# Optimization experiments

Measured on AMD Instinct MI355X. Metric: run time of the kernel, lower is better.

## Reference

```python
import jax, jax.numpy as jnp
import numpy as np

EPS = 1e-6

def setup_inputs() -> dict:
    key = jax.random.key(0)
    k1, k2, k3 = jax.random.split(key, 3)
    B, D, V = 8, 4096, 32000
    hidden_states = jax.random.normal(k1, (B, D), dtype=jnp.float32)
    norm_weight = jax.random.normal(k2, (D,), dtype=jnp.float32)
    lm_head_weight = jax.random.normal(k3, (V, D), dtype=jnp.float32) * (D ** -0.5)
    return {"hidden_states": hidden_states, "norm_weight": norm_weight,
            "lm_head_weight": lm_head_weight}

def reference(hidden_states, norm_weight, lm_head_weight):
    # RMSNorm: x * rsqrt(mean(x^2) + eps) * gamma
    var = jnp.mean(jnp.square(hidden_states), axis=-1, keepdims=True)
    h = hidden_states * jax.lax.rsqrt(var + EPS) * norm_weight  # [B, D]
    # vocab projection (GEMV per row): logits [B, V]
    logits = jnp.einsum('bd,vd->bv', h, lm_head_weight)
    # top-1 token, matching torch.topk(logits.float(), 1) -> indices [B, 1]
    token = jnp.argmax(logits.astype(jnp.float32), axis=-1, keepdims=True)
    return token
```

## Files before the change

kernel.cpp:

```cpp
#include <hip/hip_runtime.h>
#include <stdint.h>


#define D 4096
#define BATCH 8
#define VOCAB 32000
#define VT 4
#define NGROUPS (VOCAB / VT)
#define NBLK 2000
#define EPS 1e-6f

typedef unsigned long long u64;
typedef float f32x4 __attribute__((ext_vector_type(4)));

__global__ __launch_bounds__(256) void rmsnorm_k(const float* __restrict__ x,
                                                 const float* __restrict__ g,
                                                 float* __restrict__ h) {
    const int b = blockIdx.x;
    const int t = threadIdx.x;
    const int wave = t >> 6, lane = t & 63;
    const float* xr = x + b * D;

    f32x4 xv[4];
    float s = 0.f;
#pragma unroll
    for (int i = 0; i < 4; ++i) {
        xv[i] = *(const f32x4*)(xr + i * 1024 + t * 4);
        s += xv[i].x * xv[i].x + xv[i].y * xv[i].y + xv[i].z * xv[i].z + xv[i].w * xv[i].w;
    }
#pragma unroll
    for (int m = 1; m < 64; m <<= 1) s += __shfl_xor(s, m, 64);

    __shared__ float wsum[4];
    if (lane == 0) wsum[wave] = s;
    __syncthreads();
    const float tot = wsum[0] + wsum[1] + wsum[2] + wsum[3];
    const float rs = rsqrtf(tot * (1.f / (float)D) + EPS);

#pragma unroll
    for (int i = 0; i < 4; ++i) {
        const int d = i * 1024 + t * 4;
        const f32x4 gv = *(const f32x4*)(g + d);
        f32x4 o;
        o.x = xv[i].x * rs * gv.x;
        o.y = xv[i].y * rs * gv.y;
        o.z = xv[i].z * rs * gv.z;
        o.w = xv[i].w * rs * gv.w;
        *(f32x4*)(h + b * D + d) = o;
    }
}

__global__ __launch_bounds__(256) void gemv_argmax_k(const float* __restrict__ W,
                                                     const float* __restrict__ h,
                                                     u64* __restrict__ partial) {
    const int lane = threadIdx.x & 63;
    const int wave = threadIdx.x >> 6;
    const int grp = blockIdx.x * 4 + wave;
    const int v0 = grp * VT;
    const float* Wb = W + (size_t)v0 * D;

    float acc[32];
#pragma unroll
    for (int i = 0; i < 32; ++i) acc[i] = 0.f;

    f32x4 bufA[VT], bufB[VT];
    const int dl = lane * 4;

#define LOADW(BUF, c)                                                           \
    {                                                                           \
        const int _d = (c) * 256 + dl;                                          \
        _Pragma("unroll")                                                       \
        for (int vi = 0; vi < VT; ++vi)                                         \
            BUF[vi] = __builtin_nontemporal_load((const f32x4*)(Wb + vi * D + _d)); \
    }

#define COMPUTE(BUF, c)                                                         \
    {                                                                           \
        const int _d = (c) * 256 + dl;                                          \
        _Pragma("unroll")                                                       \
        for (int b = 0; b < 8; ++b) {                                           \
            const f32x4 hv = *(const f32x4*)(h + b * D + _d);                   \
            _Pragma("unroll")                                                   \
            for (int vi = 0; vi < VT; ++vi)                                     \
                acc[b * VT + vi] += BUF[vi].x * hv.x + BUF[vi].y * hv.y +       \
                                    BUF[vi].z * hv.z + BUF[vi].w * hv.w;        \
        }                                                                       \
    }

    LOADW(bufA, 0)
#pragma unroll 1
    for (int c = 0; c < 16; c += 2) {
        LOADW(bufB, c + 1)
        COMPUTE(bufA, c)
        LOADW(bufA, (c + 2 < 16 ? c + 2 : 15))
        COMPUTE(bufB, c + 1)
    }
#undef LOADW
#undef COMPUTE

#pragma unroll
    for (int s = 0; s < 5; ++s) {
        const int m = 1 << s;
        const bool bit = (lane & m) != 0;
#pragma unroll
        for (int u = 0; u < (32 >> (s + 1)); ++u) {
            const float a = acc[2 * u];
            const float c2 = acc[2 * u + 1];
            const float keep = bit ? c2 : a;
            const float send = bit ? a : c2;
            acc[u] = keep + __shfl_xor(send, m, 64);
        }
    }
    float logit = acc[0] + __shfl_xor(acc[0], 32, 64);

    const int vidx = v0 + (lane & 3);
    const uint32_t fb = __float_as_uint(logit);
    const uint32_t key = (fb & 0x80000000u) ? ~fb : (fb | 0x80000000u);
    u64 best = ((u64)key << 32) | (uint32_t)(~(uint32_t)vidx);

#pragma unroll
    for (int m = 1; m <= 2; m <<= 1) {
        const u64 o = __shfl_xor(best, m, 64);
        if (o > best) best = o;
    }
    {
        const u64 o = __shfl_xor(best, 32, 64);
        if (o > best) best = o;
    }

    __shared__ u64 lb[4][8];
    if (lane < 32 && (lane & 3) == 0) lb[wave][lane >> 2] = best;
    __syncthreads();
    if (threadIdx.x < 8) {
        const u64 m0 = lb[0][threadIdx.x], m1 = lb[1][threadIdx.x];
        const u64 m2 = lb[2][threadIdx.x], m3 = lb[3][threadIdx.x];
        const u64 a = m0 > m1 ? m0 : m1;
        const u64 b2 = m2 > m3 ? m2 : m3;
        partial[(size_t)blockIdx.x * 8 + threadIdx.x] = a > b2 ? a : b2;
    }
}

__global__ __launch_bounds__(512) void finalize_k(const u64* __restrict__ partial,
                                                  int* __restrict__ out, int nblk) {
    const int b = threadIdx.x >> 6;
    const int lane = threadIdx.x & 63;
    u64 best = 0ull;
    for (int p = lane; p < nblk; p += 64) {
        const u64 x = partial[(size_t)p * 8 + b];
        if (x > best) best = x;
    }
#pragma unroll
    for (int m = 1; m < 64; m <<= 1) {
        const u64 o = __shfl_xor(best, m, 64);
        if (o > best) best = o;
    }
    if (lane == 0) out[b] = (int)(~(uint32_t)best);
}

extern "C" void kernel_launch(void* const* d_in, const int* in_sizes, int n_in,
                              void* d_out, int out_size, void* d_ws, size_t ws_size,
                              hipStream_t stream) {
    const float* x = (const float*)d_in[0];
    const float* g = (const float*)d_in[1];
    const float* W = (const float*)d_in[2];
    int* out = (int*)d_out;

    float* h = (float*)d_ws;
    u64* partial = (u64*)((char*)d_ws + BATCH * D * sizeof(float));

    rmsnorm_k<<<BATCH, 256, 0, stream>>>(x, g, h);
    gemv_argmax_k<<<NBLK, 256, 0, stream>>>(W, h, partial);
    finalize_k<<<1, 512, 0, stream>>>(partial, out, NBLK);
}
```

Baseline: 135.8 us.

## Make GEMV-argmax persistent with 1024-thread blocks and hidden states staged in LDS

Replaces the 2000-block, one-group-per-wave launch with 256 persistent blocks of 16 waves. Each wave loops over vocab groups in a grid-stride pattern and keeps a running best (logit, index). Each block first copies all 8×4096 normalized hidden states (128 KB) into shared memory so the inner product reads h from LDS instead of global/L2. The cost is a large per-block LDS copy and only one block per CU. The __launch_bounds__(1024, 4) hint asks for far more resident waves than the LDS allows, which may squeeze the register budget and cause spills.

```diff
diff --git a/kernel.cpp b/kernel.cpp
--- a/kernel.cpp
+++ b/kernel.cpp
@@ -7,7 +7,9 @@
 #define VOCAB 32000
 #define VT 4
 #define NGROUPS (VOCAB / VT)
-#define NBLK 2000
+#define NBLK 256
+#define WPB 16
+#define NWAVES (NBLK * WPB)
 #define EPS 1e-6f
 
 typedef unsigned long long u64;
@@ -50,73 +52,93 @@
     }
 }
 
-__global__ __launch_bounds__(256) void gemv_argmax_k(const float* __restrict__ W,
-                                                     const float* __restrict__ h,
-                                                     u64* __restrict__ partial) {
-    const int lane = threadIdx.x & 63;
-    const int wave = threadIdx.x >> 6;
-    const int grp = blockIdx.x * 4 + wave;
-    const int v0 = grp * VT;
-    const float* Wb = W + (size_t)v0 * D;
+__global__ __launch_bounds__(1024, 4) void gemv_argmax_k(const float* __restrict__ W,
+                                                         const float* __restrict__ h,
+                                                         u64* __restrict__ partial) {
+    extern __shared__ float hs[];
+    const int t = threadIdx.x;
 
-    float acc[32];
+    {
+        const f32x4* src = (const f32x4*)h;
+        f32x4* dst = (f32x4*)hs;
 #pragma unroll
-    for (int i = 0; i < 32; ++i) acc[i] = 0.f;
+        for (int i = 0; i < 8; ++i) dst[i * 1024 + t] = src[i * 1024 + t];
+    }
+    __syncthreads();
+
+    const int lane = t & 63;
+    const int wave = t >> 6;
+    const int wid = blockIdx.x * WPB + wave;
+    const int dl = lane * 4;
+
+    u64 best = 0ull;
 
     f32x4 bufA[VT], bufB[VT];
-    const int dl = lane * 4;
 
-#define LOADW(BUF, c)                                                           \
-    {                                                                           \
-        const int _d = (c) * 256 + dl;                                          \
-        _Pragma("unroll")                                                       \
-        for (int vi = 0; vi < VT; ++vi)                                         \
-            BUF[vi] = __builtin_nontemporal_load((const f32x4*)(Wb + vi * D + _d)); \
+#define LOADW(BUF, WB, c)                                                          \
+    {                                                                              \
+        const int _d = (c) * 256 + dl;                                             \
+        _Pragma("unroll")                                                          \
+        for (int vi = 0; vi < VT; ++vi)                                            \
+            BUF[vi] = __builtin_nontemporal_load((const f32x4*)((WB) + vi * D + _d)); \
     }
 
-#define COMPUTE(BUF, c)                                                         \
-    {                                                                           \
-        const int _d = (c) * 256 + dl;                                          \
-        _Pragma("unroll")                                                       \
-        for (int b = 0; b < 8; ++b) {                                           \
-            const f32x4 hv = *(const f32x4*)(h + b * D + _d);                   \
-            _Pragma("unroll")                                                   \
-            for (int vi = 0; vi < VT; ++vi)                                     \
-                acc[b * VT + vi] += BUF[vi].x * hv.x + BUF[vi].y * hv.y +       \
-                                    BUF[vi].z * hv.z + BUF[vi].w * hv.w;        \
-        }                                                                       \
+#define COMPUTE(BUF, c)                                                            \
+    {                                                                              \
+        const int _d = (c) * 256 + dl;                                             \
+        _Pragma("unroll")                                                          \
+        for (int b = 0; b < 8; ++b) {                                              \
+            const f32x4 hv = *(const f32x4*)(hs + b * D + _d);                     \
+            _Pragma("unroll")                                                      \
+            for (int vi = 0; vi < VT; ++vi)                                        \
+                acc[b * VT + vi] += BUF[vi].x * hv.x + BUF[vi].y * hv.y +          \
+                                    BUF[vi].z * hv.z + BUF[vi].w * hv.w;           \
+        }                                                                          \
     }
 
-    LOADW(bufA, 0)
 #pragma unroll 1
-    for (int c = 0; c < 16; c += 2) {
-        LOADW(bufB, c + 1)
-        COMPUTE(bufA, c)
-        LOADW(bufA, (c + 2 < 16 ? c + 2 : 15))
-        COMPUTE(bufB, c + 1)
+    for (int grp = wid; grp < NGROUPS; grp += NWAVES) {
+        const float* Wb = W + (size_t)grp * (VT * D);
+
+        float acc[32];
+#pragma unroll
+        for (int i = 0; i < 32; ++i) acc[i] = 0.f;
+
+        LOADW(bufA, Wb, 0)
+#pragma unroll 1
+        for (int c = 0; c <= 12; c += 2) {
+            LOADW(bufB, Wb, c + 1)
+            COMPUTE(bufA, c)
+            LOADW(bufA, Wb, c + 2)
+            COMPUTE(bufB, c + 1)
+        }
+        LOADW(bufB, Wb, 15)
+        COMPUTE(bufA, 14)
+        COMPUTE(bufB, 15)
+
+#pragma unroll
+        for (int s = 0; s < 5; ++s) {
+            const int m = 1 << s;
+            const bool bit = (lane & m) != 0;
+#pragma unroll
+            for (int u = 0; u < (32 >> (s + 1)); ++u) {
+                const float a = acc[2 * u];
+                const float c2 = acc[2 * u + 1];
+                const float keep = bit ? c2 : a;
+                const float send = bit ? a : c2;
+                acc[u] = keep + __shfl_xor(send, m, 64);
+            }
+        }
+        const float logit = acc[0] + __shfl_xor(acc[0], 32, 64);
+
+        const int vidx = grp * VT + (lane & 3);
+        const uint32_t fb = __float_as_uint(logit);
+        const uint32_t key = (fb & 0x80000000u) ? ~fb : (fb | 0x80000000u);
+        const u64 pk = ((u64)key << 32) | (uint32_t)(~(uint32_t)vidx);
+        if (pk > best) best = pk;
     }
 #undef LOADW
 #undef COMPUTE
-
-#pragma unroll
-    for (int s = 0; s < 5; ++s) {
-        const int m = 1 << s;
-        const bool bit = (lane & m) != 0;
-#pragma unroll
-        for (int u = 0; u < (32 >> (s + 1)); ++u) {
-            const float a = acc[2 * u];
-            const float c2 = acc[2 * u + 1];
-            const float keep = bit ? c2 : a;
-            const float send = bit ? a : c2;
-            acc[u] = keep + __shfl_xor(send, m, 64);
-        }
-    }
-    float logit = acc[0] + __shfl_xor(acc[0], 32, 64);
-
-    const int vidx = v0 + (lane & 3);
-    const uint32_t fb = __float_as_uint(logit);
-    const uint32_t key = (fb & 0x80000000u) ? ~fb : (fb | 0x80000000u);
-    u64 best = ((u64)key << 32) | (uint32_t)(~(uint32_t)vidx);
 
 #pragma unroll
     for (int m = 1; m <= 2; m <<= 1) {
@@ -128,15 +150,17 @@
         if (o > best) best = o;
     }
 
-    __shared__ u64 lb[4][8];
+    __shared__ u64 lb[WPB][8];
     if (lane < 32 && (lane & 3) == 0) lb[wave][lane >> 2] = best;
     __syncthreads();
-    if (threadIdx.x < 8) {
-        const u64 m0 = lb[0][threadIdx.x], m1 = lb[1][threadIdx.x];
-        const u64 m2 = lb[2][threadIdx.x], m3 = lb[3][threadIdx.x];
-        const u64 a = m0 > m1 ? m0 : m1;
-        const u64 b2 = m2 > m3 ? m2 : m3;
-        partial[(size_t)blockIdx.x * 8 + threadIdx.x] = a > b2 ? a : b2;
+    if (t < 8) {
+        u64 m = lb[0][t];
+#pragma unroll
+        for (int w2 = 1; w2 < WPB; ++w2) {
+            const u64 o = lb[w2][t];
+            if (o > m) m = o;
+        }
+        partial[(size_t)blockIdx.x * 8 + t] = m;
     }
 }
 
@@ -169,6 +193,6 @@
     u64* partial = (u64*)((char*)d_ws + BATCH * D * sizeof(float));
 
     rmsnorm_k<<<BATCH, 256, 0, stream>>>(x, g, h);
-    gemv_argmax_k<<<NBLK, 256, 0, stream>>>(W, h, partial);
+    gemv_argmax_k<<<NBLK, 1024, BATCH * D * sizeof(float), stream>>>(W, h, partial);
     finalize_k<<<1, 512, 0, stream>>>(partial, out, NBLK);
 }
```

Result: slower. 149.8 us (+10.3%).

## Split GEMV over D into four slices with LDS-cached hidden states

Applied to the files above, without the earlier changes.

Splits the reduction dimension into four 1024-column slices per block, caches the matching slice of the normalized hidden states in shared memory, and has each wave process eight groups of four vocab rows. Per-slice partial logits are written to a workspace, and a new finalize kernel (one block per batch row) sums the four slices and performs the argmax. This replaces repeated global/L2 reads of h with LDS reads and shrinks the grid. In exchange it writes and rereads roughly 1 MB of partial logits, and the finalize kernel runs on only eight blocks.

```diff
diff --git a/kernel.cpp b/kernel.cpp
--- a/kernel.cpp
+++ b/kernel.cpp
@@ -6,8 +6,10 @@
 #define BATCH 8
 #define VOCAB 32000
 #define VT 4
-#define NGROUPS (VOCAB / VT)
-#define NBLK 2000
+#define SLICES 4
+#define BPS 250
+#define NBLKB (SLICES * BPS)
+#define GPW 8
 #define EPS 1e-6f
 
 typedef unsigned long long u64;
@@ -50,36 +52,43 @@
     }
 }
 
-__global__ __launch_bounds__(256) void gemv_argmax_k(const float* __restrict__ W,
-                                                     const float* __restrict__ h,
-                                                     u64* __restrict__ partial) {
-    const int lane = threadIdx.x & 63;
-    const int wave = threadIdx.x >> 6;
-    const int grp = blockIdx.x * 4 + wave;
-    const int v0 = grp * VT;
-    const float* Wb = W + (size_t)v0 * D;
+__global__ __launch_bounds__(256, 4) void gemv_slice_k(const float* __restrict__ W,
+                                                       const float* __restrict__ h,
+                                                       float* __restrict__ partial) {
+    __shared__ float hs[BATCH][1024];
+    const int bid = blockIdx.x;
+    const int s = bid & 3;
+    const int t = threadIdx.x;
+    const int lane = t & 63, wave = t >> 6;
+    const int scol = s * 1024;
+
+#pragma unroll
+    for (int r = 0; r < BATCH; ++r)
+        *(f32x4*)&hs[r][t * 4] = *(const f32x4*)(h + r * D + scol + t * 4);
+    __syncthreads();
+
+    const int wsub = (bid >> 2) * 4 + wave;
+    const int dl = lane * 4;
 
     float acc[32];
 #pragma unroll
     for (int i = 0; i < 32; ++i) acc[i] = 0.f;
 
-    f32x4 bufA[VT], bufB[VT];
-    const int dl = lane * 4;
-
-#define LOADW(BUF, c)                                                           \
+    f32x4 wA[VT], wB[VT];
+
+#define LOADW(BUF, WGP, c)                                                      \
     {                                                                           \
-        const int _d = (c) * 256 + dl;                                          \
         _Pragma("unroll")                                                       \
         for (int vi = 0; vi < VT; ++vi)                                         \
-            BUF[vi] = __builtin_nontemporal_load((const f32x4*)(Wb + vi * D + _d)); \
+            BUF[vi] = __builtin_nontemporal_load(                               \
+                (const f32x4*)((WGP) + (size_t)vi * D + (c) * 256));            \
     }
 
 #define COMPUTE(BUF, c)                                                         \
     {                                                                           \
-        const int _d = (c) * 256 + dl;                                          \
-        _Pragma("unroll")                                                       \
-        for (int b = 0; b < 8; ++b) {                                           \
-            const f32x4 hv = *(const f32x4*)(h + b * D + _d);                   \
+        _Pragma("unroll")                                                       \
+        for (int b = 0; b < BATCH; ++b) {                                       \
+            const f32x4 hv = *(const f32x4*)(&hs[b][(c) * 256 + dl]);           \
             _Pragma("unroll")                                                   \
             for (int vi = 0; vi < VT; ++vi)                                     \
                 acc[b * VT + vi] += BUF[vi].x * hv.x + BUF[vi].y * hv.y +       \
@@ -87,74 +96,93 @@
         }                                                                       \
     }
 
-    LOADW(bufA, 0)
+#define FLUSH(g)                                                                \
+    {                                                                           \
+        _Pragma("unroll")                                                       \
+        for (int st = 0; st < 5; ++st) {                                        \
+            const int m = 1 << st;                                              \
+            const bool bit = (lane & m) != 0;                                   \
+            _Pragma("unroll")                                                   \
+            for (int u = 0; u < (32 >> (st + 1)); ++u) {                        \
+                const float a0 = acc[2 * u], a1 = acc[2 * u + 1];               \
+                const float keep = bit ? a1 : a0;                               \
+                const float send = bit ? a0 : a1;                               \
+                acc[u] = keep + __shfl_xor(send, m, 64);                        \
+            }                                                                   \
+        }                                                                       \
+        const float logit = acc[0] + __shfl_xor(acc[0], 32, 64);                \
+        if (lane < 32) {                                                        \
+            const int b_ = lane >> 2, vi_ = lane & 3;                           \
+            const int v_ = (wsub * GPW + (g)) * VT + vi_;                       \
+            partial[(size_t)(s * BATCH + b_) * VOCAB + v_] = logit;             \
+        }                                                                       \
+        _Pragma("unroll")                                                       \
+        for (int i2 = 0; i2 < 32; ++i2) acc[i2] = 0.f;                          \
+    }
+
+    const float* Wg = W + (size_t)(wsub * 32) * D + scol + dl;
+
+    LOADW(wA, Wg, 0)
 #pragma unroll 1
-    for (int c = 0; c < 16; c += 2) {
-        LOADW(bufB, c + 1)
-        COMPUTE(bufA, c)
-        LOADW(bufA, (c + 2 < 16 ? c + 2 : 15))
-        COMPUTE(bufB, c + 1)
-    }
+    for (int g = 0; g < GPW - 1; ++g) {
+        LOADW(wB, Wg, 1)
+        COMPUTE(wA, 0)
+        LOADW(wA, Wg, 2)
+        COMPUTE(wB, 1)
+        LOADW(wB, Wg, 3)
+        COMPUTE(wA, 2)
+        const float* Wn = Wg + (size_t)VT * D;
+        LOADW(wA, Wn, 0)
+        COMPUTE(wB, 3)
+        FLUSH(g)
+        Wg = Wn;
+    }
+    LOADW(wB, Wg, 1)
+    COMPUTE(wA, 0)
+    LOADW(wA, Wg, 2)
+    COMPUTE(wB, 1)
+    LOADW(wB, Wg, 3)
+    COMPUTE(wA, 2)
+    COMPUTE(wB, 3)
+    FLUSH(GPW - 1)
 #undef LOADW
 #undef COMPUTE
-
-#pragma unroll
-    for (int s = 0; s < 5; ++s) {
-        const int m = 1 << s;
-        const bool bit = (lane & m) != 0;
-#pragma unroll
-        for (int u = 0; u < (32 >> (s + 1)); ++u) {
-            const float a = acc[2 * u];
-            const float c2 = acc[2 * u + 1];
-            const float keep = bit ? c2 : a;
-            const float send = bit ? a : c2;
-            acc[u] = keep + __shfl_xor(send, m, 64);
-        }
-    }
-    float logit = acc[0] + __shfl_xor(acc[0], 32, 64);
-
-    const int vidx = v0 + (lane & 3);
-    const uint32_t fb = __float_as_uint(logit);
-    const uint32_t key = (fb & 0x80000000u) ? ~fb : (fb | 0x80000000u);
-    u64 best = ((u64)key << 32) | (uint32_t)(~(uint32_t)vidx);
-
-#pragma unroll
-    for (int m = 1; m <= 2; m <<= 1) {
-        const u64 o = __shfl_xor(best, m, 64);
-        if (o > best) best = o;
-    }
-    {
-        const u64 o = __shfl_xor(best, 32, 64);
-        if (o > best) best = o;
-    }
-
-    __shared__ u64 lb[4][8];
-    if (lane < 32 && (lane & 3) == 0) lb[wave][lane >> 2] = best;
-    __syncthreads();
-    if (threadIdx.x < 8) {
-        const u64 m0 = lb[0][threadIdx.x], m1 = lb[1][threadIdx.x];
-        const u64 m2 = lb[2][threadIdx.x], m3 = lb[3][threadIdx.x];
-        const u64 a = m0 > m1 ? m0 : m1;
-        const u64 b2 = m2 > m3 ? m2 : m3;
-        partial[(size_t)blockIdx.x * 8 + threadIdx.x] = a > b2 ? a : b2;
-    }
-}
-
-__global__ __launch_bounds__(512) void finalize_k(const u64* __restrict__ partial,
-                                                  int* __restrict__ out, int nblk) {
-    const int b = threadIdx.x >> 6;
-    const int lane = threadIdx.x & 63;
+#undef FLUSH
+}
+
+__global__ __launch_bounds__(1024) void finalize_k(const float* __restrict__ partial,
+                                                   int* __restrict__ out) {
+    const int b = blockIdx.x;
+    const int t = threadIdx.x;
+    const int lane = t & 63, wave = t >> 6;
+    const float* p0 = partial + (size_t)(0 * BATCH + b) * VOCAB;
+    const float* p1 = partial + (size_t)(1 * BATCH + b) * VOCAB;
+    const float* p2 = partial + (size_t)(2 * BATCH + b) * VOCAB;
+    const float* p3 = partial + (size_t)(3 * BATCH + b) * VOCAB;
+
     u64 best = 0ull;
-    for (int p = lane; p < nblk; p += 64) {
-        const u64 x = partial[(size_t)p * 8 + b];
-        if (x > best) best = x;
+    for (int v = t; v < VOCAB; v += 1024) {
+        const float sum = p0[v] + p1[v] + p2[v] + p3[v];
+        const uint32_t fb = __float_as_uint(sum);
+        const uint32_t key = (fb & 0x80000000u) ? ~fb : (fb | 0x80000000u);
+        const u64 pk = ((u64)key << 32) | (uint32_t)(~(uint32_t)v);
+        if (pk > best) best = pk;
     }
 #pragma unroll
     for (int m = 1; m < 64; m <<= 1) {
         const u64 o = __shfl_xor(best, m, 64);
         if (o > best) best = o;
     }
-    if (lane == 0) out[b] = (int)(~(uint32_t)best);
+    __shared__ u64 red[16];
+    if (lane == 0) red[wave] = best;
+    __syncthreads();
+    if (t == 0) {
+        u64 m = red[0];
+#pragma unroll
+        for (int i = 1; i < 16; ++i)
+            if (red[i] > m) m = red[i];
+        out[b] = (int)(~(uint32_t)m);
+    }
 }
 
 extern "C" void kernel_launch(void* const* d_in, const int* in_sizes, int n_in,
@@ -166,9 +194,9 @@
     int* out = (int*)d_out;
 
     float* h = (float*)d_ws;
-    u64* partial = (u64*)((char*)d_ws + BATCH * D * sizeof(float));
+    float* partial = (float*)((char*)d_ws + BATCH * D * sizeof(float));
 
     rmsnorm_k<<<BATCH, 256, 0, stream>>>(x, g, h);
-    gemv_argmax_k<<<NBLK, 256, 0, stream>>>(W, h, partial);
-    finalize_k<<<1, 512, 0, stream>>>(partial, out, NBLK);
-}
+    gemv_slice_k<<<NBLKB, 256, 0, stream>>>(W, h, partial);
+    finalize_k<<<BATCH, 1024, 0, stream>>>(partial, out);
+}
```

After: 295.4 us. 2.18x slower.
